# Performance work log

Hardware: AMD Instinct MI355X
Metric: run time of the kernel (lower is better)

Reference implementation:

```python
import jax, jax.numpy as jnp
import numpy as np

B, D, H = 16384, 1024, 1024
EPS = 1e-07


def setup_inputs() -> dict:
    key = jax.random.key(0)
    ks = jax.random.split(key, 16)
    s = 1.0 / np.sqrt(D)  # xavier-ish scale keeps exp() gate bounded
    mat = lambda k: (jax.random.normal(k, (D, H), dtype=jnp.float32) * s)
    zeros = lambda: jnp.zeros((H,), dtype=jnp.float32)
    return {
        "x": jax.random.normal(ks[0], (B, D), dtype=jnp.float32),
        "h_prev": jax.random.normal(ks[1], (B, H), dtype=jnp.float32) * 0.1,
        "c_prev": jax.random.normal(ks[2], (B, H), dtype=jnp.float32) * 0.1,
        "n_prev": jnp.ones((B, H), dtype=jnp.float32),
        "Wz": mat(ks[3]), "bWz": zeros(), "Rz": mat(ks[4]), "bRz": zeros(), "bz": zeros(),
        "Wi": mat(ks[5]), "bWi": zeros(), "Ri": mat(ks[6]), "bRi": zeros(), "bi": zeros(),
        "Wf": mat(ks[7]), "bWf": zeros(), "Rf": mat(ks[8]), "bRf": zeros(), "bf": zeros(),
        "Wo": mat(ks[9]), "bWo": zeros(), "Ro": mat(ks[10]), "bRo": zeros(), "bo": zeros(),
        "Wy": mat(ks[11]), "by": jnp.zeros((D,), dtype=jnp.float32),
    }


def reference(x, h_prev, c_prev, n_prev,
              Wz, bWz, Rz, bRz, bz,
              Wi, bWi, Ri, bRi, bi,
              Wf, bWf, Rf, bRf, bf,
              Wo, bWo, Ro, bRo, bo,
              Wy, by):
    # pre-activations: two fused GEMMs via concatenated weights
    Wcat = jnp.concatenate([Wz, Wi, Wf, Wo], axis=1)      # [D, 4H]
    Rcat = jnp.concatenate([Rz, Ri, Rf, Ro], axis=1)      # [H, 4H]
    bcat = jnp.concatenate([bWz + bRz + bz, bWi + bRi + bi,
                            bWf + bRf + bf, bWo + bRo + bo])
    pre = x @ Wcat + h_prev @ Rcat + bcat                  # [B, 4H]
    pz, pi, pf, po = jnp.split(pre, 4, axis=1)
    zt = jnp.tanh(pz)
    it = jnp.exp(pi)
    ft = jax.nn.sigmoid(pf)
    ot = jax.nn.sigmoid(po)
    C = ft * c_prev + it * zt
    n = ft * n_prev + it
    h = ot * jnp.tanh(C / (n + EPS))
    y = h @ Wy + by
    return y, (h, C, n)
```

## Files before the change

### kernel.cpp

```cpp
#include <hip/hip_runtime.h>
#include <math.h>
#include <stdint.h>


typedef __attribute__((ext_vector_type(8))) short bf16x8;
typedef __attribute__((ext_vector_type(4))) float f32x4;

constexpr int Bsz = 16384;
constexpr int Dd  = 1024;
constexpr int Hh  = 1024;
constexpr float EPSv = 1e-7f;

__device__ __forceinline__ unsigned short f2bf(float f) {
    union { float f; uint32_t u; } v; v.f = f;
    uint32_t u = v.u + 0x7fffu + ((v.u >> 16) & 1u);
    return (unsigned short)(u >> 16);
}

__device__ __forceinline__ void gload16(const void* g, void* l) {
    __builtin_amdgcn_global_load_lds(
        (const __attribute__((address_space(1))) void*)g,
        (__attribute__((address_space(3))) void*)l, 16, 0, 0);
}


__global__ __launch_bounds__(256)
void cvt_A(const float* __restrict__ x, const float* __restrict__ hp, unsigned short* __restrict__ A)
{
    const int idx = blockIdx.x * 256 + threadIdx.x;
    const int n = idx * 8;
    const int b = n >> 11, k = n & 2047;
    const float* s = (k < 1024) ? (x + (size_t)b * 1024 + k)
                                : (hp + (size_t)b * 1024 + (k - 1024));
    const float4 v0 = *(const float4*)s;
    const float4 v1 = *(const float4*)(s + 4);
    union { unsigned short u[8]; uint4 v; } pk;
    pk.u[0] = f2bf(v0.x); pk.u[1] = f2bf(v0.y); pk.u[2] = f2bf(v0.z); pk.u[3] = f2bf(v0.w);
    pk.u[4] = f2bf(v1.x); pk.u[5] = f2bf(v1.y); pk.u[6] = f2bf(v1.z); pk.u[7] = f2bf(v1.w);
    *(uint4*)(A + n) = pk.v;
}

__global__ __launch_bounds__(256)
void cvt_T(const float* __restrict__ src, unsigned short* __restrict__ dst,
           int ldd, int kbase, int g, int mode)
{
    __shared__ float tile[64][65];
    const int t = threadIdx.x;
    const int kt = blockIdx.x & 15, jt = blockIdx.x >> 4;
    {
        const int lr = t >> 4, lc = (t & 15) * 4;
        #pragma unroll
        for (int rr = 0; rr < 64; rr += 16) {
            const float4 v = *(const float4*)(src + (size_t)(kt * 64 + rr + lr) * 1024 + jt * 64 + lc);
            tile[rr + lr][lc + 0] = v.x;
            tile[rr + lr][lc + 1] = v.y;
            tile[rr + lr][lc + 2] = v.z;
            tile[rr + lr][lc + 3] = v.w;
        }
    }
    __syncthreads();
    const int jl = t >> 2, kc = (t & 3) * 16;
    const int j = jt * 64 + jl;
    const int cp = mode ? j : ((j & 15) | (g << 4) | ((j >> 4) << 6));
    union { unsigned short u[16]; uint4 v[2]; } pk;
    #pragma unroll
    for (int q = 0; q < 16; ++q) pk.u[q] = f2bf(tile[kc + q][jl]);
    uint4* d = (uint4*)(dst + (size_t)cp * ldd + kbase + kt * 64 + kc);
    d[0] = pk.v[0];
    d[1] = pk.v[1];
}

__global__ __launch_bounds__(256)
void bias_sum(const float* bWz, const float* bRz, const float* bz,
              const float* bWi, const float* bRi, const float* bi,
              const float* bWf, const float* bRf, const float* bf_,
              const float* bWo, const float* bRo, const float* bo,
              float* __restrict__ bs)
{
    const int j = blockIdx.x * 256 + threadIdx.x;
    bs[j]        = bWz[j] + bRz[j] + bz[j];
    bs[1024 + j] = bWi[j] + bRi[j] + bi[j];
    bs[2048 + j] = bWf[j] + bRf[j] + bf_[j];
    bs[3072 + j] = bWo[j] + bRo[j] + bo[j];
}


template<int LDA, int NT, int NTILES, class Epi>
__device__ void mfma_chain(const unsigned short* __restrict__ Ag,
                           const unsigned short* __restrict__ Bg,
                           int m0base, int n0, int t,
                           unsigned short* lds, Epi epi)
{
    constexpr int TOT = NT * NTILES;
    const int lane = t & 63, wid = t >> 6;
    const int wr = wid >> 2, wc = wid & 3;
    const int cl = lane & 15, hi = lane >> 4;
    const int aB = (wr * 128 + cl) * 64 + ((hi ^ (cl & 7)) << 3);
    const int bB = 16384 + (wc * 64 + cl) * 64 + ((hi ^ (cl & 7)) << 3);
    const int srow = t >> 3;
    const int schk = ((t & 7) ^ (srow & 7)) << 3;
    unsigned short* ldst = lds + t * 8;

    f32x4 acc[8][4];
    #pragma unroll
    for (int i = 0; i < 8; ++i)
        #pragma unroll
        for (int j = 0; j < 4; ++j) acc[i][j] = (f32x4)0.f;

    auto stgA = [&](int fi, int buf) {
        const int ot = fi / NT, kt = fi % NT;
        const unsigned short* g = Ag + (size_t)(m0base + ot * 256 + srow) * LDA + kt * 64 + schk;
        unsigned short* l = ldst + buf * 32768;
        gload16(g,                    l);
        gload16(g + (size_t) 64 * LDA, l + 4096);
        gload16(g + (size_t)128 * LDA, l + 8192);
        gload16(g + (size_t)192 * LDA, l + 12288);
    };
    auto stgB = [&](int fi, int buf) {
        const int kt = fi % NT;
        const unsigned short* g = Bg + (size_t)(n0 + srow) * LDA + kt * 64 + schk;
        unsigned short* l = ldst + buf * 32768 + 16384;
        gload16(g,                    l);
        gload16(g + (size_t) 64 * LDA, l + 4096);
        gload16(g + (size_t)128 * LDA, l + 8192);
        gload16(g + (size_t)192 * LDA, l + 12288);
    };

    stgA(0, 0); stgB(0, 0); stgB(1, 1);
    asm volatile("s_waitcnt vmcnt(4)" ::: "memory");
    __builtin_amdgcn_s_barrier();

    for (int fi = 0; fi < TOT; ++fi) {
        const int bufR = fi & 1;
        const unsigned short* L = lds + bufR * 32768;
        int f1 = fi + 1; if (f1 > TOT - 1) f1 = TOT - 1;
        int f2 = fi + 2; if (f2 > TOT - 1) f2 = TOT - 1;

        bf16x8 Br0[4], Br1[4], Ar00[4], Ar01[4], Ar10[4], Ar11[4];
        #pragma unroll
        for (int nn = 0; nn < 4; ++nn) Br0[nn]  = *(const bf16x8*)(L + (bB + nn * 1024));
        #pragma unroll
        for (int mm = 0; mm < 4; ++mm) Ar00[mm] = *(const bf16x8*)(L + (aB + mm * 1024));

        stgA(f1, bufR ^ 1);

        #pragma unroll
        for (int nn = 0; nn < 4; ++nn) Br1[nn]  = *(const bf16x8*)(L + ((bB + nn * 1024) ^ 32));
        #pragma unroll
        for (int mm = 0; mm < 4; ++mm) Ar01[mm] = *(const bf16x8*)(L + ((aB + mm * 1024) ^ 32));

        __builtin_amdgcn_s_setprio(1);
        #pragma unroll
        for (int mm = 0; mm < 4; ++mm)
            #pragma unroll
            for (int nn = 0; nn < 4; ++nn)
                acc[mm][nn] = __builtin_amdgcn_mfma_f32_16x16x32_bf16(Ar00[mm], Br0[nn], acc[mm][nn], 0, 0, 0);
        __builtin_amdgcn_s_setprio(0);

        #pragma unroll
        for (int mm = 0; mm < 4; ++mm) Ar10[mm] = *(const bf16x8*)(L + (aB + 4096 + mm * 1024));
        #pragma unroll
        for (int mm = 0; mm < 4; ++mm) Ar11[mm] = *(const bf16x8*)(L + ((aB + 4096 + mm * 1024) ^ 32));

        __builtin_amdgcn_s_setprio(1);
        #pragma unroll
        for (int mm = 0; mm < 4; ++mm)
            #pragma unroll
            for (int nn = 0; nn < 4; ++nn)
                acc[mm][nn] = __builtin_amdgcn_mfma_f32_16x16x32_bf16(Ar01[mm], Br1[nn], acc[mm][nn], 0, 0, 0);
        __builtin_amdgcn_s_setprio(0);

        __builtin_amdgcn_sched_barrier(0);
        __builtin_amdgcn_s_barrier();

        stgB(f2, bufR);

        __builtin_amdgcn_s_setprio(1);
        #pragma unroll
        for (int mm = 0; mm < 4; ++mm)
            #pragma unroll
            for (int nn = 0; nn < 4; ++nn)
                acc[4 + mm][nn] = __builtin_amdgcn_mfma_f32_16x16x32_bf16(Ar10[mm], Br0[nn], acc[4 + mm][nn], 0, 0, 0);
        __builtin_amdgcn_s_setprio(0);
        __builtin_amdgcn_s_setprio(1);
        #pragma unroll
        for (int mm = 0; mm < 4; ++mm)
            #pragma unroll
            for (int nn = 0; nn < 4; ++nn)
                acc[4 + mm][nn] = __builtin_amdgcn_mfma_f32_16x16x32_bf16(Ar11[mm], Br1[nn], acc[4 + mm][nn], 0, 0, 0);
        __builtin_amdgcn_s_setprio(0);

        __builtin_amdgcn_sched_barrier(0);
        asm volatile("s_waitcnt vmcnt(4)" ::: "memory");
        __builtin_amdgcn_s_barrier();

        if ((fi % NT) == NT - 1) {
            epi(fi / NT, acc);
            #pragma unroll
            for (int i = 0; i < 8; ++i)
                #pragma unroll
                for (int j = 0; j < 4; ++j) acc[i][j] = (f32x4)0.f;
        }
    }
    asm volatile("s_waitcnt vmcnt(0)" ::: "memory");
}

__global__ __launch_bounds__(512, 2)
void gemm_gates(const unsigned short* __restrict__ A, const unsigned short* __restrict__ WT,
                const float* __restrict__ bsum,
                const float* __restrict__ c_prev, const float* __restrict__ n_prev,
                float* __restrict__ out_h, float* __restrict__ out_C, float* __restrict__ out_n,
                unsigned short* __restrict__ h_bf)
{
    __shared__ unsigned short lds[65536];
    const int t = threadIdx.x;
    const int b = blockIdx.x;
    const int nb  = (b & 7) * 2 + (b >> 7);
    const int mb0 = ((b >> 3) & 15) * 4;
    const int m0base = mb0 * 256;
    const int n0 = nb * 256;

    const int lane = t & 63, wid = t >> 6;
    const int wr = wid >> 2, wc = wid & 3;
    const int cl = lane & 15, hi = lane >> 4;
    const int j_out = nb * 64 + wc * 16 + cl;
    const float bz_ = bsum[j_out];
    const float bi_ = bsum[1024 + j_out];
    const float bf_ = bsum[2048 + j_out];
    const float bo_ = bsum[3072 + j_out];

    auto epi = [&](int ot, f32x4 (&acc)[8][4]) {
        #pragma unroll
        for (int mf = 0; mf < 8; ++mf) {
            const int rb = m0base + ot * 256 + wr * 128 + mf * 16 + hi * 4;
            #pragma unroll
            for (int r = 0; r < 4; ++r) {
                const size_t idx = (size_t)(rb + r) * 1024 + j_out;
                const float pz = acc[mf][0][r] + bz_;
                const float pi = acc[mf][1][r] + bi_;
                const float pf = acc[mf][2][r] + bf_;
                const float po = acc[mf][3][r] + bo_;
                const float zt = tanhf(pz);
                const float it = expf(pi);
                const float ft = 1.f / (1.f + expf(-pf));
                const float ot_ = 1.f / (1.f + expf(-po));
                const float Cv = ft * c_prev[idx] + it * zt;
                const float nv = ft * n_prev[idx] + it;
                const float hv = ot_ * tanhf(Cv / (nv + EPSv));
                out_h[idx] = hv;
                out_C[idx] = Cv;
                out_n[idx] = nv;
                h_bf[idx] = f2bf(hv);
            }
        }
    };

    mfma_chain<2048, 32, 4>(A, WT, m0base, n0, t, lds, epi);
}

__global__ __launch_bounds__(512, 2)
void gemm_y(const unsigned short* __restrict__ A, const unsigned short* __restrict__ WyT,
            const float* __restrict__ by, float* __restrict__ y)
{
    __shared__ unsigned short lds[65536];
    const int t = threadIdx.x;
    const int b = blockIdx.x;
    const int nb = b & 3, mb = b >> 2;
    const int m0base = mb * 256, n0 = nb * 256;

    const int lane = t & 63, wid = t >> 6;
    const int wr = wid >> 2, wc = wid & 3;
    const int cl = lane & 15, hi = lane >> 4;

    auto epi = [&](int ot, f32x4 (&acc)[8][4]) {
        (void)ot;
        #pragma unroll
        for (int mf = 0; mf < 8; ++mf) {
            const int rb = m0base + wr * 128 + mf * 16 + hi * 4;
            #pragma unroll
            for (int nf = 0; nf < 4; ++nf) {
                const int c = n0 + wc * 64 + nf * 16 + cl;
                const float bc = by[c];
                #pragma unroll
                for (int r = 0; r < 4; ++r)
                    y[(size_t)(rb + r) * 1024 + c] = acc[mf][nf][r] + bc;
            }
        }
    };

    mfma_chain<1024, 16, 1>(A, WyT, m0base, n0, t, lds, epi);
}


constexpr int FBM = 64, FBN = 64, FBK = 16, FPAD = 4;

__global__ __launch_bounds__(256)
void fb_gates(const float* __restrict__ x, const float* __restrict__ h_prev,
              const float* __restrict__ c_prev, const float* __restrict__ n_prev,
              const float* __restrict__ Wz, const float* __restrict__ Rz,
              const float* __restrict__ Wi, const float* __restrict__ Ri,
              const float* __restrict__ Wf, const float* __restrict__ Rf,
              const float* __restrict__ Wo, const float* __restrict__ Ro,
              const float* __restrict__ bWz, const float* __restrict__ bRz, const float* __restrict__ bz,
              const float* __restrict__ bWi, const float* __restrict__ bRi, const float* __restrict__ bi,
              const float* __restrict__ bWf, const float* __restrict__ bRf, const float* __restrict__ bf_,
              const float* __restrict__ bWo, const float* __restrict__ bRo, const float* __restrict__ bo,
              float* __restrict__ out_h, float* __restrict__ out_C, float* __restrict__ out_n)
{
    __shared__ float sA[FBK][FBM + FPAD];
    __shared__ float sB[4][FBK][FBN + FPAD];
    const int t = threadIdx.x;
    const int col_blk = blockIdx.x & 15, row_blk = blockIdx.x >> 4;
    const int row0 = row_blk * FBM, col0 = col_blk * FBN;
    const int tx = t & 15, ty = t >> 4;
    float acc[4][4][4];
    #pragma unroll
    for (int g = 0; g < 4; ++g)
        for (int i = 0; i < 4; ++i)
            for (int j = 0; j < 4; ++j) acc[g][i][j] = 0.f;
    const int ar = t >> 2, ak = (t & 3) * 4, wk = t >> 4, wcc = (t & 15) * 4;
    for (int phase = 0; phase < 2; ++phase) {
        const float* Am = phase ? h_prev : x;
        const float* W0 = phase ? Rz : Wz; const float* W1 = phase ? Ri : Wi;
        const float* W2 = phase ? Rf : Wf; const float* W3 = phase ? Ro : Wo;
        for (int k0 = 0; k0 < 1024; k0 += FBK) {
            __syncthreads();
            {
                const float4 v = *(const float4*)(Am + (size_t)(row0 + ar) * 1024 + k0 + ak);
                sA[ak + 0][ar] = v.x; sA[ak + 1][ar] = v.y;
                sA[ak + 2][ar] = v.z; sA[ak + 3][ar] = v.w;
            }
            *(float4*)&sB[0][wk][wcc] = *(const float4*)(W0 + (size_t)(k0 + wk) * 1024 + col0 + wcc);
            *(float4*)&sB[1][wk][wcc] = *(const float4*)(W1 + (size_t)(k0 + wk) * 1024 + col0 + wcc);
            *(float4*)&sB[2][wk][wcc] = *(const float4*)(W2 + (size_t)(k0 + wk) * 1024 + col0 + wcc);
            *(float4*)&sB[3][wk][wcc] = *(const float4*)(W3 + (size_t)(k0 + wk) * 1024 + col0 + wcc);
            __syncthreads();
            #pragma unroll
            for (int kk = 0; kk < FBK; ++kk) {
                float a[4], bb[4][4];
                *(float4*)a = *(const float4*)&sA[kk][ty * 4];
                *(float4*)&bb[0][0] = *(const float4*)&sB[0][kk][tx * 4];
                *(float4*)&bb[1][0] = *(const float4*)&sB[1][kk][tx * 4];
                *(float4*)&bb[2][0] = *(const float4*)&sB[2][kk][tx * 4];
                *(float4*)&bb[3][0] = *(const float4*)&sB[3][kk][tx * 4];
                #pragma unroll
                for (int g = 0; g < 4; ++g)
                    for (int i = 0; i < 4; ++i)
                        for (int j = 0; j < 4; ++j)
                            acc[g][i][j] += a[i] * bb[g][j];
            }
        }
    }
    #pragma unroll
    for (int i = 0; i < 4; ++i) {
        const int r = row0 + ty * 4 + i;
        #pragma unroll
        for (int j = 0; j < 4; ++j) {
            const int c = col0 + tx * 4 + j;
            const float pz = acc[0][i][j] + bWz[c] + bRz[c] + bz[c];
            const float pi = acc[1][i][j] + bWi[c] + bRi[c] + bi[c];
            const float pf = acc[2][i][j] + bWf[c] + bRf[c] + bf_[c];
            const float po = acc[3][i][j] + bWo[c] + bRo[c] + bo[c];
            const float zt = tanhf(pz);
            const float it = expf(pi);
            const float ft = 1.f / (1.f + expf(-pf));
            const float ot = 1.f / (1.f + expf(-po));
            const size_t idx = (size_t)r * Hh + c;
            const float Cv = ft * c_prev[idx] + it * zt;
            const float nv = ft * n_prev[idx] + it;
            out_h[idx] = ot * tanhf(Cv / (nv + EPSv));
            out_C[idx] = Cv;
            out_n[idx] = nv;
        }
    }
}

__global__ __launch_bounds__(256)
void fb_ygemm(const float* __restrict__ hmat, const float* __restrict__ Wy,
              const float* __restrict__ by, float* __restrict__ y)
{
    __shared__ float sA[FBK][FBM + FPAD];
    __shared__ float sB[FBK][FBN + FPAD];
    const int t = threadIdx.x;
    const int col_blk = blockIdx.x & 15, row_blk = blockIdx.x >> 4;
    const int row0 = row_blk * FBM, col0 = col_blk * FBN;
    const int tx = t & 15, ty = t >> 4;
    float acc[4][4];
    #pragma unroll
    for (int i = 0; i < 4; ++i)
        for (int j = 0; j < 4; ++j) acc[i][j] = 0.f;
    const int ar = t >> 2, ak = (t & 3) * 4, wk = t >> 4, wcc = (t & 15) * 4;
    for (int k0 = 0; k0 < 1024; k0 += FBK) {
        __syncthreads();
        {
            const float4 v = *(const float4*)(hmat + (size_t)(row0 + ar) * 1024 + k0 + ak);
            sA[ak + 0][ar] = v.x; sA[ak + 1][ar] = v.y;
            sA[ak + 2][ar] = v.z; sA[ak + 3][ar] = v.w;
        }
        *(float4*)&sB[wk][wcc] = *(const float4*)(Wy + (size_t)(k0 + wk) * 1024 + col0 + wcc);
        __syncthreads();
        #pragma unroll
        for (int kk = 0; kk < FBK; ++kk) {
            float a[4], bb[4];
            *(float4*)a = *(const float4*)&sA[kk][ty * 4];
            *(float4*)bb = *(const float4*)&sB[kk][tx * 4];
            #pragma unroll
            for (int i = 0; i < 4; ++i)
                for (int j = 0; j < 4; ++j)
                    acc[i][j] += a[i] * bb[j];
        }
    }
    #pragma unroll
    for (int i = 0; i < 4; ++i) {
        const int r = row0 + ty * 4 + i;
        #pragma unroll
        for (int j = 0; j < 4; ++j) {
            const int c = col0 + tx * 4 + j;
            y[(size_t)r * Dd + c] = acc[i][j] + by[c];
        }
    }
}


extern "C" void kernel_launch(void* const* d_in, const int* in_sizes, int n_in,
                              void* d_out, int out_size, void* d_ws, size_t ws_size,
                              hipStream_t stream) {
    const float* x      = (const float*)d_in[0];
    const float* h_prev = (const float*)d_in[1];
    const float* c_prev = (const float*)d_in[2];
    const float* n_prev = (const float*)d_in[3];
    const float* Wz  = (const float*)d_in[4];
    const float* bWz = (const float*)d_in[5];
    const float* Rz  = (const float*)d_in[6];
    const float* bRz = (const float*)d_in[7];
    const float* bz  = (const float*)d_in[8];
    const float* Wi  = (const float*)d_in[9];
    const float* bWi = (const float*)d_in[10];
    const float* Ri  = (const float*)d_in[11];
    const float* bRi = (const float*)d_in[12];
    const float* bi  = (const float*)d_in[13];
    const float* Wf  = (const float*)d_in[14];
    const float* bWf = (const float*)d_in[15];
    const float* Rf  = (const float*)d_in[16];
    const float* bRf = (const float*)d_in[17];
    const float* bf_ = (const float*)d_in[18];
    const float* Wo  = (const float*)d_in[19];
    const float* bWo = (const float*)d_in[20];
    const float* Ro  = (const float*)d_in[21];
    const float* bRo = (const float*)d_in[22];
    const float* bo  = (const float*)d_in[23];
    const float* Wy  = (const float*)d_in[24];
    const float* by  = (const float*)d_in[25];

    float* y     = (float*)d_out;
    float* out_h = y + (size_t)Bsz * Dd;
    float* out_C = out_h + (size_t)Bsz * Hh;
    float* out_n = out_C + (size_t)Bsz * Hh;

    const size_t OFF_A    = 0;
    const size_t OFF_WT   = 67108864;
    const size_t OFF_WYT  = 83886080;
    const size_t OFF_HBF  = 85983232;
    const size_t OFF_BS   = 119537664;
    const size_t WS_NEED  = 119554048;

    if (ws_size >= WS_NEED) {
        char* ws = (char*)d_ws;
        unsigned short* A_bf = (unsigned short*)(ws + OFF_A);
        unsigned short* WT   = (unsigned short*)(ws + OFF_WT);
        unsigned short* WyT  = (unsigned short*)(ws + OFF_WYT);
        unsigned short* h_bf = (unsigned short*)(ws + OFF_HBF);
        float* bsum          = (float*)(ws + OFF_BS);

        cvt_A<<<16384, 256, 0, stream>>>(x, h_prev, A_bf);
        cvt_T<<<256, 256, 0, stream>>>(Wz, WT, 2048, 0,    0, 0);
        cvt_T<<<256, 256, 0, stream>>>(Rz, WT, 2048, 1024, 0, 0);
        cvt_T<<<256, 256, 0, stream>>>(Wi, WT, 2048, 0,    1, 0);
        cvt_T<<<256, 256, 0, stream>>>(Ri, WT, 2048, 1024, 1, 0);
        cvt_T<<<256, 256, 0, stream>>>(Wf, WT, 2048, 0,    2, 0);
        cvt_T<<<256, 256, 0, stream>>>(Rf, WT, 2048, 1024, 2, 0);
        cvt_T<<<256, 256, 0, stream>>>(Wo, WT, 2048, 0,    3, 0);
        cvt_T<<<256, 256, 0, stream>>>(Ro, WT, 2048, 1024, 3, 0);
        cvt_T<<<256, 256, 0, stream>>>(Wy, WyT, 1024, 0,   0, 1);
        bias_sum<<<4, 256, 0, stream>>>(bWz, bRz, bz, bWi, bRi, bi,
                                        bWf, bRf, bf_, bWo, bRo, bo, bsum);

        gemm_gates<<<256, 512, 0, stream>>>(A_bf, WT, bsum, c_prev, n_prev,
                                            out_h, out_C, out_n, h_bf);
        gemm_y<<<256, 512, 0, stream>>>(h_bf, WyT, by, y);
    } else {
        dim3 block(256);
        dim3 grid((Bsz / FBM) * (Hh / FBN));
        fb_gates<<<grid, block, 0, stream>>>(x, h_prev, c_prev, n_prev,
                                             Wz, Rz, Wi, Ri, Wf, Rf, Wo, Ro,
                                             bWz, bRz, bz, bWi, bRi, bi,
                                             bWf, bRf, bf_, bWo, bRo, bo,
                                             out_h, out_C, out_n);
        fb_ygemm<<<grid, block, 0, stream>>>(out_h, Wy, by, y);
    }
}
```

Baseline: 451.4 us.

## Switch GEMM core to 32x32x16 MFMA with triple-buffered B tiles

Replaces the 16x16x32 bf16 MFMA mainloop with a 32x32x16 variant. The wave layout changes to 4x2, each wave owns a 64x128 tile, and the gate-weight column permutation and epilogue indexing are updated to match. B tiles are now triple-buffered in a larger LDS allocation. The loop is split into four barrier-delimited phases that interleave LDS reads, global-to-LDS prefetch and MFMA bursts, and the gate epilogue uses __expf-based tanh and sigmoid. The goal is fewer LDS reads per FLOP and higher MFMA throughput. The cost is more LDS per block, which may hurt occupancy, more barriers, and slightly lower-precision transcendentals.

```diff
diff --git a/kernel.cpp b/kernel.cpp
--- a/kernel.cpp
+++ b/kernel.cpp
@@ -5,6 +5,7 @@
 
 typedef __attribute__((ext_vector_type(8))) short bf16x8;
 typedef __attribute__((ext_vector_type(4))) float f32x4;
+typedef __attribute__((ext_vector_type(16))) float f32x16;
 
 constexpr int Bsz = 16384;
 constexpr int Dd  = 1024;
@@ -21,6 +22,14 @@
     __builtin_amdgcn_global_load_lds(
         (const __attribute__((address_space(1))) void*)g,
         (__attribute__((address_space(3))) void*)l, 16, 0, 0);
+}
+
+__device__ __forceinline__ float sigm_f(float x) { return 1.f / (1.f + __expf(-x)); }
+__device__ __forceinline__ float tanh_f(float x) {
+    const float ax = fabsf(x);
+    const float t = __expf(-2.f * ax);
+    const float r = (1.f - t) / (1.f + t);
+    return copysignf(r, x);
 }
 
 
@@ -61,7 +70,7 @@
     __syncthreads();
     const int jl = t >> 2, kc = (t & 3) * 16;
     const int j = jt * 64 + jl;
-    const int cp = mode ? j : ((j & 15) | (g << 4) | ((j >> 4) << 6));
+    const int cp = mode ? j : ((j & 31) | (g << 5) | ((j >> 5) << 7));
     union { unsigned short u[16]; uint4 v[2]; } pk;
     #pragma unroll
     for (int q = 0; q < 16; ++q) pk.u[q] = f2bf(tile[kc + q][jl]);
@@ -85,122 +94,127 @@
 }
 
 
-template<int LDA, int NT, int NTILES, class Epi>
-__device__ void mfma_chain(const unsigned short* __restrict__ Ag,
-                           const unsigned short* __restrict__ Bg,
-                           int m0base, int n0, int t,
-                           unsigned short* lds, Epi epi)
-{
-    constexpr int TOT = NT * NTILES;
+#define PH_PRE() { __builtin_amdgcn_sched_barrier(0); __builtin_amdgcn_s_barrier(); \
+    asm volatile("s_waitcnt lgkmcnt(0)" ::: "memory"); __builtin_amdgcn_sched_barrier(0); \
+    __builtin_amdgcn_s_setprio(1); }
+#define PH_POST() { __builtin_amdgcn_s_setprio(0); __builtin_amdgcn_sched_barrier(0); \
+    __builtin_amdgcn_s_barrier(); }
+#define MFMA32(d, a, b) d = __builtin_amdgcn_mfma_f32_32x32x16_bf16(a, b, d, 0, 0, 0)
+
+template<int LD, int NTK_LOG2, int NTILES, class Epi>
+__device__ void mfma32_chain(const unsigned short* __restrict__ Ag,
+                             const unsigned short* __restrict__ Bg,
+                             int m0base, int n0, int t,
+                             unsigned short* lds, Epi epi)
+{
+    constexpr int NTK = 1 << NTK_LOG2;
+    constexpr int TOT = NTK * NTILES;
     const int lane = t & 63, wid = t >> 6;
-    const int wr = wid >> 2, wc = wid & 3;
-    const int cl = lane & 15, hi = lane >> 4;
-    const int aB = (wr * 128 + cl) * 64 + ((hi ^ (cl & 7)) << 3);
-    const int bB = 16384 + (wc * 64 + cl) * 64 + ((hi ^ (cl & 7)) << 3);
+    const int wr = wid >> 1, wc = wid & 1;
+    const int l31 = lane & 31, hi5 = lane >> 5, e7 = l31 & 7;
+    const int rA0 = wr * 64 + l31;
+    const int rB0 = wc * 128 + l31;
     const int srow = t >> 3;
-    const int schk = ((t & 7) ^ (srow & 7)) << 3;
-    unsigned short* ldst = lds + t * 8;
-
-    f32x4 acc[8][4];
+    const int schk = ((t & 7) ^ (srow & 7)) * 8;
+    const int ldst8 = t * 8;
+
+    f32x16 acc[2][4];
     #pragma unroll
-    for (int i = 0; i < 8; ++i)
-        #pragma unroll
-        for (int j = 0; j < 4; ++j) acc[i][j] = (f32x4)0.f;
-
-    auto stgA = [&](int fi, int buf) {
-        const int ot = fi / NT, kt = fi % NT;
-        const unsigned short* g = Ag + (size_t)(m0base + ot * 256 + srow) * LDA + kt * 64 + schk;
-        unsigned short* l = ldst + buf * 32768;
-        gload16(g,                    l);
-        gload16(g + (size_t) 64 * LDA, l + 4096);
-        gload16(g + (size_t)128 * LDA, l + 8192);
-        gload16(g + (size_t)192 * LDA, l + 12288);
+    for (int i = 0; i < 2; ++i)
+        #pragma unroll
+        for (int j = 0; j < 4; ++j) acc[i][j] = (f32x16)0.f;
+
+    auto stgA = [&](int f, int h, int buf) {
+        const int ot = f >> NTK_LOG2, kt = f & (NTK - 1);
+        const unsigned short* g = Ag + (size_t)(m0base + ot * 256 + h * 128 + srow) * LD + kt * 64 + schk;
+        unsigned short* l = lds + buf * 16384 + h * 8192 + ldst8;
+        gload16(g,                 l);
+        gload16(g + (size_t)64 * LD, l + 4096);
     };
-    auto stgB = [&](int fi, int buf) {
-        const int kt = fi % NT;
-        const unsigned short* g = Bg + (size_t)(n0 + srow) * LDA + kt * 64 + schk;
-        unsigned short* l = ldst + buf * 32768 + 16384;
-        gload16(g,                    l);
-        gload16(g + (size_t) 64 * LDA, l + 4096);
-        gload16(g + (size_t)128 * LDA, l + 8192);
-        gload16(g + (size_t)192 * LDA, l + 12288);
+    auto stgB = [&](int f, int h, int buf) {
+        const int kt = f & (NTK - 1);
+        const unsigned short* g = Bg + (size_t)(n0 + h * 128 + srow) * LD + kt * 64 + schk;
+        unsigned short* l = lds + 32768 + buf * 16384 + h * 8192 + ldst8;
+        gload16(g,                 l);
+        gload16(g + (size_t)64 * LD, l + 4096);
     };
-
-    stgA(0, 0); stgB(0, 0); stgB(1, 1);
+    auto rdA = [&](int buf, int mi, int ks) {
+        return *(const bf16x8*)(lds + buf * 16384 + (rA0 + mi * 32) * 64 + ((((ks << 1) + hi5) ^ e7) << 3));
+    };
+    auto rdB = [&](int buf, int nn, int ks) {
+        return *(const bf16x8*)(lds + 32768 + buf * 16384 + (rB0 + nn * 32) * 64 + ((((ks << 1) + hi5) ^ e7) << 3));
+    };
+
+    stgA(0, 0, 0); stgA(0, 1, 0);
+    stgB(0, 0, 0); stgB(0, 1, 0);
+    stgB(1, 0, 1); stgB(1, 1, 1);
     asm volatile("s_waitcnt vmcnt(4)" ::: "memory");
     __builtin_amdgcn_s_barrier();
 
-    for (int fi = 0; fi < TOT; ++fi) {
-        const int bufR = fi & 1;
-        const unsigned short* L = lds + bufR * 32768;
-        int f1 = fi + 1; if (f1 > TOT - 1) f1 = TOT - 1;
-        int f2 = fi + 2; if (f2 > TOT - 1) f2 = TOT - 1;
-
-        bf16x8 Br0[4], Br1[4], Ar00[4], Ar01[4], Ar10[4], Ar11[4];
-        #pragma unroll
-        for (int nn = 0; nn < 4; ++nn) Br0[nn]  = *(const bf16x8*)(L + (bB + nn * 1024));
-        #pragma unroll
-        for (int mm = 0; mm < 4; ++mm) Ar00[mm] = *(const bf16x8*)(L + (aB + mm * 1024));
-
-        stgA(f1, bufR ^ 1);
-
-        #pragma unroll
-        for (int nn = 0; nn < 4; ++nn) Br1[nn]  = *(const bf16x8*)(L + ((bB + nn * 1024) ^ 32));
-        #pragma unroll
-        for (int mm = 0; mm < 4; ++mm) Ar01[mm] = *(const bf16x8*)(L + ((aB + mm * 1024) ^ 32));
-
-        __builtin_amdgcn_s_setprio(1);
-        #pragma unroll
-        for (int mm = 0; mm < 4; ++mm)
-            #pragma unroll
-            for (int nn = 0; nn < 4; ++nn)
-                acc[mm][nn] = __builtin_amdgcn_mfma_f32_16x16x32_bf16(Ar00[mm], Br0[nn], acc[mm][nn], 0, 0, 0);
+    int bB = 0;
+    for (int f = 0; f < TOT; ++f) {
+        const int bA = f & 1;
+        int f1 = f + 1; if (f1 > TOT - 1) f1 = TOT - 1;
+        int f2 = f + 2; if (f2 > TOT - 1) f2 = TOT - 1;
+        const int bB2 = (bB >= 1) ? (bB - 1) : 2;
+
+        bf16x8 a00, a01, a10, a11, b00, b01, b10, b11, c00, c01, c10, c11;
+
+        a00 = rdA(bA, 0, 0); a10 = rdA(bA, 1, 0);
+        a01 = rdA(bA, 0, 1); a11 = rdA(bA, 1, 1);
+        b00 = rdB(bB, 0, 0); b10 = rdB(bB, 1, 0);
+        b01 = rdB(bB, 0, 1); b11 = rdB(bB, 1, 1);
+        stgA(f1, 0, bA ^ 1);
+        PH_PRE();
+        MFMA32(acc[0][0], a00, b00); MFMA32(acc[1][0], a10, b00);
+        MFMA32(acc[0][1], a00, b10); MFMA32(acc[1][1], a10, b10);
+        MFMA32(acc[0][0], a01, b01); MFMA32(acc[1][0], a11, b01);
+        MFMA32(acc[0][1], a01, b11); MFMA32(acc[1][1], a11, b11);
+        PH_POST();
+
+        c00 = rdB(bB, 2, 0); c10 = rdB(bB, 3, 0);
+        c01 = rdB(bB, 2, 1); c11 = rdB(bB, 3, 1);
+        stgA(f1, 1, bA ^ 1);
+        PH_PRE();
+        MFMA32(acc[0][2], a00, c00); MFMA32(acc[1][2], a10, c00);
+        MFMA32(acc[0][3], a00, c10); MFMA32(acc[1][3], a10, c10);
+        MFMA32(acc[0][2], a01, c01); MFMA32(acc[1][2], a11, c01);
+        MFMA32(acc[0][3], a01, c11); MFMA32(acc[1][3], a11, c11);
+        PH_POST();
+
+        a00 = rdA(bA, 0, 2); a10 = rdA(bA, 1, 2);
+        a01 = rdA(bA, 0, 3); a11 = rdA(bA, 1, 3);
+        b00 = rdB(bB, 0, 2); b10 = rdB(bB, 1, 2);
+        b01 = rdB(bB, 0, 3); b11 = rdB(bB, 1, 3);
+        stgB(f2, 0, bB2);
+        PH_PRE();
+        MFMA32(acc[0][0], a00, b00); MFMA32(acc[1][0], a10, b00);
+        MFMA32(acc[0][1], a00, b10); MFMA32(acc[1][1], a10, b10);
+        MFMA32(acc[0][0], a01, b01); MFMA32(acc[1][0], a11, b01);
+        MFMA32(acc[0][1], a01, b11); MFMA32(acc[1][1], a11, b11);
+        PH_POST();
+
+        c00 = rdB(bB, 2, 2); c10 = rdB(bB, 3, 2);
+        c01 = rdB(bB, 2, 3); c11 = rdB(bB, 3, 3);
+        stgB(f2, 1, bB2);
+        PH_PRE();
+        MFMA32(acc[0][2], a00, c00); MFMA32(acc[1][2], a10, c00);
+        MFMA32(acc[0][3], a00, c10); MFMA32(acc[1][3], a10, c10);
+        MFMA32(acc[0][2], a01, c01); MFMA32(acc[1][2], a11, c01);
+        MFMA32(acc[0][3], a01, c11); MFMA32(acc[1][3], a11, c11);
         __builtin_amdgcn_s_setprio(0);
-
-        #pragma unroll
-        for (int mm = 0; mm < 4; ++mm) Ar10[mm] = *(const bf16x8*)(L + (aB + 4096 + mm * 1024));
-        #pragma unroll
-        for (int mm = 0; mm < 4; ++mm) Ar11[mm] = *(const bf16x8*)(L + ((aB + 4096 + mm * 1024) ^ 32));
-
-        __builtin_amdgcn_s_setprio(1);
-        #pragma unroll
-        for (int mm = 0; mm < 4; ++mm)
-            #pragma unroll
-            for (int nn = 0; nn < 4; ++nn)
-                acc[mm][nn] = __builtin_amdgcn_mfma_f32_16x16x32_bf16(Ar01[mm], Br1[nn], acc[mm][nn], 0, 0, 0);
-        __builtin_amdgcn_s_setprio(0);
-
-        __builtin_amdgcn_sched_barrier(0);
-        __builtin_amdgcn_s_barrier();
-
-        stgB(f2, bufR);
-
-        __builtin_amdgcn_s_setprio(1);
-        #pragma unroll
-        for (int mm = 0; mm < 4; ++mm)
-            #pragma unroll
-            for (int nn = 0; nn < 4; ++nn)
-                acc[4 + mm][nn] = __builtin_amdgcn_mfma_f32_16x16x32_bf16(Ar10[mm], Br0[nn], acc[4 + mm][nn], 0, 0, 0);
-        __builtin_amdgcn_s_setprio(0);
-        __builtin_amdgcn_s_setprio(1);
-        #pragma unroll
-        for (int mm = 0; mm < 4; ++mm)
-            #pragma unroll
-            for (int nn = 0; nn < 4; ++nn)
-                acc[4 + mm][nn] = __builtin_amdgcn_mfma_f32_16x16x32_bf16(Ar11[mm], Br1[nn], acc[4 + mm][nn], 0, 0, 0);
-        __builtin_amdgcn_s_setprio(0);
-
         __builtin_amdgcn_sched_barrier(0);
         asm volatile("s_waitcnt vmcnt(4)" ::: "memory");
         __builtin_amdgcn_s_barrier();
 
-        if ((fi % NT) == NT - 1) {
-            epi(fi / NT, acc);
+        if ((f & (NTK - 1)) == NTK - 1) {
+            epi(f >> NTK_LOG2, acc);
             #pragma unroll
-            for (int i = 0; i < 8; ++i)
+            for (int i = 0; i < 2; ++i)
                 #pragma unroll
-                for (int j = 0; j < 4; ++j) acc[i][j] = (f32x4)0.f;
-        }
+                for (int j = 0; j < 4; ++j) acc[i][j] = (f32x16)0.f;
+        }
+        bB = (bB == 2) ? 0 : bB + 1;
     }
     asm volatile("s_waitcnt vmcnt(0)" ::: "memory");
 }
@@ -212,7 +226,7 @@
                 float* __restrict__ out_h, float* __restrict__ out_C, float* __restrict__ out_n,
                 unsigned short* __restrict__ h_bf)
 {
-    __shared__ unsigned short lds[65536];
+    __shared__ unsigned short lds[81920];
     const int t = threadIdx.x;
     const int b = blockIdx.x;
     const int nb  = (b & 7) * 2 + (b >> 7);
@@ -221,32 +235,33 @@
     const int n0 = nb * 256;
 
     const int lane = t & 63, wid = t >> 6;
-    const int wr = wid >> 2, wc = wid & 3;
-    const int cl = lane & 15, hi = lane >> 4;
-    const int j_out = nb * 64 + wc * 16 + cl;
+    const int wr = wid >> 1, wc = wid & 1;
+    const int l31 = lane & 31, hi5 = lane >> 5;
+    const int j_out = (nb * 2 + wc) * 32 + l31;
     const float bz_ = bsum[j_out];
     const float bi_ = bsum[1024 + j_out];
     const float bf_ = bsum[2048 + j_out];
     const float bo_ = bsum[3072 + j_out];
 
-    auto epi = [&](int ot, f32x4 (&acc)[8][4]) {
-        #pragma unroll
-        for (int mf = 0; mf < 8; ++mf) {
-            const int rb = m0base + ot * 256 + wr * 128 + mf * 16 + hi * 4;
+    auto epi = [&](int ot, f32x16 (&acc)[2][4]) {
+        #pragma unroll
+        for (int mi = 0; mi < 2; ++mi) {
+            const int rbase = m0base + ot * 256 + wr * 64 + mi * 32 + 4 * hi5;
             #pragma unroll
-            for (int r = 0; r < 4; ++r) {
-                const size_t idx = (size_t)(rb + r) * 1024 + j_out;
-                const float pz = acc[mf][0][r] + bz_;
-                const float pi = acc[mf][1][r] + bi_;
-                const float pf = acc[mf][2][r] + bf_;
-                const float po = acc[mf][3][r] + bo_;
-                const float zt = tanhf(pz);
-                const float it = expf(pi);
-                const float ft = 1.f / (1.f + expf(-pf));
-                const float ot_ = 1.f / (1.f + expf(-po));
+            for (int r = 0; r < 16; ++r) {
+                const int row = rbase + (r & 3) + 8 * (r >> 2);
+                const size_t idx = (size_t)row * 1024 + j_out;
+                const float pz = acc[mi][0][r] + bz_;
+                const float pi = acc[mi][1][r] + bi_;
+                const float pf = acc[mi][2][r] + bf_;
+                const float po = acc[mi][3][r] + bo_;
+                const float zt = tanh_f(pz);
+                const float it = __expf(pi);
+                const float ft = sigm_f(pf);
+                const float ot_ = sigm_f(po);
                 const float Cv = ft * c_prev[idx] + it * zt;
                 const float nv = ft * n_prev[idx] + it;
-                const float hv = ot_ * tanhf(Cv / (nv + EPSv));
+                const float hv = ot_ * tanh_f(Cv / (nv + EPSv));
                 out_h[idx] = hv;
                 out_C[idx] = Cv;
                 out_n[idx] = nv;
@@ -255,40 +270,42 @@
         }
     };
 
-    mfma_chain<2048, 32, 4>(A, WT, m0base, n0, t, lds, epi);
+    mfma32_chain<2048, 5, 4>(A, WT, m0base, n0, t, lds, epi);
 }
 
 __global__ __launch_bounds__(512, 2)
 void gemm_y(const unsigned short* __restrict__ A, const unsigned short* __restrict__ WyT,
             const float* __restrict__ by, float* __restrict__ y)
 {
-    __shared__ unsigned short lds[65536];
+    __shared__ unsigned short lds[81920];
     const int t = threadIdx.x;
     const int b = blockIdx.x;
     const int nb = b & 3, mb = b >> 2;
     const int m0base = mb * 256, n0 = nb * 256;
 
     const int lane = t & 63, wid = t >> 6;
-    const int wr = wid >> 2, wc = wid & 3;
-    const int cl = lane & 15, hi = lane >> 4;
-
-    auto epi = [&](int ot, f32x4 (&acc)[8][4]) {
+    const int wr = wid >> 1, wc = wid & 1;
+    const int l31 = lane & 31, hi5 = lane >> 5;
+
+    auto epi = [&](int ot, f32x16 (&acc)[2][4]) {
         (void)ot;
         #pragma unroll
-        for (int mf = 0; mf < 8; ++mf) {
-            const int rb = m0base + wr * 128 + mf * 16 + hi * 4;
+        for (int mi = 0; mi < 2; ++mi) {
+            const int rbase = m0base + wr * 64 + mi * 32 + 4 * hi5;
             #pragma unroll
-            for (int nf = 0; nf < 4; ++nf) {
-                const int c = n0 + wc * 64 + nf * 16 + cl;
+            for (int nn = 0; nn < 4; ++nn) {
+                const int c = n0 + wc * 128 + nn * 32 + l31;
                 const float bc = by[c];
                 #pragma unroll
-                for (int r = 0; r < 4; ++r)
-                    y[(size_t)(rb + r) * 1024 + c] = acc[mf][nf][r] + bc;
+                for (int r = 0; r < 16; ++r) {
+                    const int row = rbase + (r & 3) + 8 * (r >> 2);
+                    y[(size_t)row * 1024 + c] = acc[mi][nn][r] + bc;
+                }
             }
         }
     };
 
-    mfma_chain<1024, 16, 1>(A, WyT, m0base, n0, t, lds, epi);
+    mfma32_chain<1024, 4, 1>(A, WyT, m0base, n0, t, lds, epi);
 }
 
 
```

Result: slower. 468.1 us (+3.7%).

## Restructure MFMA mainloop with triple-buffered B tiles and fast transcendental epilogue

Applied to the files above, without the earlier changes.

Rewrites the GEMM core loop so the A tile is double-buffered and the B tile triple-buffered, with one barrier per iteration, prefetches issued at the top, and a simpler load-then-MFMA sequence without priority hints. LDS grows to 160KB per block. The gate epilogue also swaps tanhf/expf for __expf-based fast sigmoid and tanh approximations. The larger LDS footprint may reduce occupancy below the declared two blocks per CU, and the simpler schedule loses the hand-tuned interleaving of LDS reads with MFMAs.

```diff
diff --git a/kernel.cpp b/kernel.cpp
--- a/kernel.cpp
+++ b/kernel.cpp
@@ -21,6 +21,14 @@
     __builtin_amdgcn_global_load_lds(
         (const __attribute__((address_space(1))) void*)g,
         (__attribute__((address_space(3))) void*)l, 16, 0, 0);
+}
+
+__device__ __forceinline__ float sigm_f(float x) { return 1.f / (1.f + __expf(-x)); }
+__device__ __forceinline__ float tanh_f(float x) {
+    const float ax = fabsf(x);
+    const float t = __expf(-2.f * ax);
+    const float r = (1.f - t) / (1.f + t);
+    return copysignf(r, x);
 }
 
 
@@ -85,21 +93,41 @@
 }
 
 
-template<int LDA, int NT, int NTILES, class Epi>
-__device__ void mfma_chain(const unsigned short* __restrict__ Ag,
-                           const unsigned short* __restrict__ Bg,
-                           int m0base, int n0, int t,
-                           unsigned short* lds, Epi epi)
-{
-    constexpr int TOT = NT * NTILES;
+template<int LD, int NTK, int NTILES, class Epi>
+__device__ void mfma_core(const unsigned short* __restrict__ Ag,
+                          const unsigned short* __restrict__ Bg,
+                          int m0base, int n0, int t,
+                          unsigned short* lds, Epi epi)
+{
+    constexpr int TOT = NTK * NTILES;
     const int lane = t & 63, wid = t >> 6;
     const int wr = wid >> 2, wc = wid & 3;
     const int cl = lane & 15, hi = lane >> 4;
-    const int aB = (wr * 128 + cl) * 64 + ((hi ^ (cl & 7)) << 3);
-    const int bB = 16384 + (wc * 64 + cl) * 64 + ((hi ^ (cl & 7)) << 3);
+    char* const L = (char*)lds;
+    const int rdA0 = (wr * 128 + cl) * 128 + ((hi ^ (cl & 7)) << 4);
+    const int rdB0 = 65536 + (wc * 64 + cl) * 128 + ((hi ^ (cl & 7)) << 4);
     const int srow = t >> 3;
-    const int schk = ((t & 7) ^ (srow & 7)) << 3;
-    unsigned short* ldst = lds + t * 8;
+    const int schk = ((t & 7) ^ (srow & 7)) * 8;
+    const int sdst = t * 16;
+
+    auto stgA = [&](int f, int buf) {
+        const int ot = f / NTK, kt = f % NTK;
+        const unsigned short* g = Ag + (size_t)(m0base + ot * 256 + srow) * LD + kt * 64 + schk;
+        char* d = L + buf * 32768 + sdst;
+        gload16(g,                  d);
+        gload16(g + (size_t) 64 * LD, d + 8192);
+        gload16(g + (size_t)128 * LD, d + 16384);
+        gload16(g + (size_t)192 * LD, d + 24576);
+    };
+    auto stgB = [&](int f, int buf) {
+        const int kt = f % NTK;
+        const unsigned short* g = Bg + (size_t)(n0 + srow) * LD + kt * 64 + schk;
+        char* d = L + 65536 + buf * 32768 + sdst;
+        gload16(g,                  d);
+        gload16(g + (size_t) 64 * LD, d + 8192);
+        gload16(g + (size_t)128 * LD, d + 16384);
+        gload16(g + (size_t)192 * LD, d + 24576);
+    };
 
     f32x4 acc[8][4];
     #pragma unroll
@@ -107,100 +135,52 @@
         #pragma unroll
         for (int j = 0; j < 4; ++j) acc[i][j] = (f32x4)0.f;
 
-    auto stgA = [&](int fi, int buf) {
-        const int ot = fi / NT, kt = fi % NT;
-        const unsigned short* g = Ag + (size_t)(m0base + ot * 256 + srow) * LDA + kt * 64 + schk;
-        unsigned short* l = ldst + buf * 32768;
-        gload16(g,                    l);
-        gload16(g + (size_t) 64 * LDA, l + 4096);
-        gload16(g + (size_t)128 * LDA, l + 8192);
-        gload16(g + (size_t)192 * LDA, l + 12288);
-    };
-    auto stgB = [&](int fi, int buf) {
-        const int kt = fi % NT;
-        const unsigned short* g = Bg + (size_t)(n0 + srow) * LDA + kt * 64 + schk;
-        unsigned short* l = ldst + buf * 32768 + 16384;
-        gload16(g,                    l);
-        gload16(g + (size_t) 64 * LDA, l + 4096);
-        gload16(g + (size_t)128 * LDA, l + 8192);
-        gload16(g + (size_t)192 * LDA, l + 12288);
-    };
-
     stgA(0, 0); stgB(0, 0); stgB(1, 1);
-    asm volatile("s_waitcnt vmcnt(4)" ::: "memory");
-    __builtin_amdgcn_s_barrier();
-
-    for (int fi = 0; fi < TOT; ++fi) {
-        const int bufR = fi & 1;
-        const unsigned short* L = lds + bufR * 32768;
-        int f1 = fi + 1; if (f1 > TOT - 1) f1 = TOT - 1;
-        int f2 = fi + 2; if (f2 > TOT - 1) f2 = TOT - 1;
-
-        bf16x8 Br0[4], Br1[4], Ar00[4], Ar01[4], Ar10[4], Ar11[4];
-        #pragma unroll
-        for (int nn = 0; nn < 4; ++nn) Br0[nn]  = *(const bf16x8*)(L + (bB + nn * 1024));
-        #pragma unroll
-        for (int mm = 0; mm < 4; ++mm) Ar00[mm] = *(const bf16x8*)(L + (aB + mm * 1024));
-
-        stgA(f1, bufR ^ 1);
-
-        #pragma unroll
-        for (int nn = 0; nn < 4; ++nn) Br1[nn]  = *(const bf16x8*)(L + ((bB + nn * 1024) ^ 32));
-        #pragma unroll
-        for (int mm = 0; mm < 4; ++mm) Ar01[mm] = *(const bf16x8*)(L + ((aB + mm * 1024) ^ 32));
-
-        __builtin_amdgcn_s_setprio(1);
-        #pragma unroll
-        for (int mm = 0; mm < 4; ++mm)
-            #pragma unroll
-            for (int nn = 0; nn < 4; ++nn)
-                acc[mm][nn] = __builtin_amdgcn_mfma_f32_16x16x32_bf16(Ar00[mm], Br0[nn], acc[mm][nn], 0, 0, 0);
-        __builtin_amdgcn_s_setprio(0);
-
-        #pragma unroll
-        for (int mm = 0; mm < 4; ++mm) Ar10[mm] = *(const bf16x8*)(L + (aB + 4096 + mm * 1024));
-        #pragma unroll
-        for (int mm = 0; mm < 4; ++mm) Ar11[mm] = *(const bf16x8*)(L + ((aB + 4096 + mm * 1024) ^ 32));
-
-        __builtin_amdgcn_s_setprio(1);
-        #pragma unroll
-        for (int mm = 0; mm < 4; ++mm)
-            #pragma unroll
-            for (int nn = 0; nn < 4; ++nn)
-                acc[mm][nn] = __builtin_amdgcn_mfma_f32_16x16x32_bf16(Ar01[mm], Br1[nn], acc[mm][nn], 0, 0, 0);
-        __builtin_amdgcn_s_setprio(0);
-
-        __builtin_amdgcn_sched_barrier(0);
+
+    int bA = 0, bB = 0;
+    for (int f = 0; f < TOT; ++f) {
+        const int f1 = (f + 1 < TOT) ? f + 1 : TOT - 1;
+        const int f2 = (f + 2 < TOT) ? f + 2 : TOT - 1;
+        const int bB2 = (bB >= 1) ? bB - 1 : 2;
+
         __builtin_amdgcn_s_barrier();
-
-        stgB(f2, bufR);
-
-        __builtin_amdgcn_s_setprio(1);
-        #pragma unroll
-        for (int mm = 0; mm < 4; ++mm)
-            #pragma unroll
-            for (int nn = 0; nn < 4; ++nn)
-                acc[4 + mm][nn] = __builtin_amdgcn_mfma_f32_16x16x32_bf16(Ar10[mm], Br0[nn], acc[4 + mm][nn], 0, 0, 0);
-        __builtin_amdgcn_s_setprio(0);
-        __builtin_amdgcn_s_setprio(1);
-        #pragma unroll
-        for (int mm = 0; mm < 4; ++mm)
-            #pragma unroll
-            for (int nn = 0; nn < 4; ++nn)
-                acc[4 + mm][nn] = __builtin_amdgcn_mfma_f32_16x16x32_bf16(Ar11[mm], Br1[nn], acc[4 + mm][nn], 0, 0, 0);
-        __builtin_amdgcn_s_setprio(0);
-
-        __builtin_amdgcn_sched_barrier(0);
-        asm volatile("s_waitcnt vmcnt(4)" ::: "memory");
-        __builtin_amdgcn_s_barrier();
-
-        if ((fi % NT) == NT - 1) {
-            epi(fi / NT, acc);
+        stgA(f1, bA ^ 1);
+        stgB(f2, bB2);
+        asm volatile("s_waitcnt vmcnt(12)" ::: "memory");
+
+        const int aof = rdA0 + (bA << 15);
+        const int bof = rdB0 + (bB << 15);
+        bf16x8 a[8], b[4];
+
+        #pragma unroll
+        for (int mf = 0; mf < 8; ++mf) a[mf] = *(const bf16x8*)(L + aof + mf * 2048);
+        #pragma unroll
+        for (int nf = 0; nf < 4; ++nf) b[nf] = *(const bf16x8*)(L + bof + nf * 2048);
+        #pragma unroll
+        for (int mf = 0; mf < 8; ++mf)
+            #pragma unroll
+            for (int nf = 0; nf < 4; ++nf)
+                acc[mf][nf] = __builtin_amdgcn_mfma_f32_16x16x32_bf16(a[mf], b[nf], acc[mf][nf], 0, 0, 0);
+
+        #pragma unroll
+        for (int mf = 0; mf < 8; ++mf) a[mf] = *(const bf16x8*)(L + (aof ^ 64) + mf * 2048);
+        #pragma unroll
+        for (int nf = 0; nf < 4; ++nf) b[nf] = *(const bf16x8*)(L + (bof ^ 64) + nf * 2048);
+        #pragma unroll
+        for (int mf = 0; mf < 8; ++mf)
+            #pragma unroll
+            for (int nf = 0; nf < 4; ++nf)
+                acc[mf][nf] = __builtin_amdgcn_mfma_f32_16x16x32_bf16(a[mf], b[nf], acc[mf][nf], 0, 0, 0);
+
+        if ((f % NTK) == NTK - 1) {
+            epi(f / NTK, acc);
             #pragma unroll
             for (int i = 0; i < 8; ++i)
                 #pragma unroll
                 for (int j = 0; j < 4; ++j) acc[i][j] = (f32x4)0.f;
         }
+        bA ^= 1;
+        bB = (bB == 2) ? 0 : bB + 1;
     }
     asm volatile("s_waitcnt vmcnt(0)" ::: "memory");
 }
@@ -212,7 +192,7 @@
                 float* __restrict__ out_h, float* __restrict__ out_C, float* __restrict__ out_n,
                 unsigned short* __restrict__ h_bf)
 {
-    __shared__ unsigned short lds[65536];
+    __shared__ unsigned short lds[81920];
     const int t = threadIdx.x;
     const int b = blockIdx.x;
     const int nb  = (b & 7) * 2 + (b >> 7);
@@ -240,13 +220,13 @@
                 const float pi = acc[mf][1][r] + bi_;
                 const float pf = acc[mf][2][r] + bf_;
                 const float po = acc[mf][3][r] + bo_;
-                const float zt = tanhf(pz);
-                const float it = expf(pi);
-                const float ft = 1.f / (1.f + expf(-pf));
-                const float ot_ = 1.f / (1.f + expf(-po));
+                const float zt = tanh_f(pz);
+                const float it = __expf(pi);
+                const float ft = sigm_f(pf);
+                const float ot_ = sigm_f(po);
                 const float Cv = ft * c_prev[idx] + it * zt;
                 const float nv = ft * n_prev[idx] + it;
-                const float hv = ot_ * tanhf(Cv / (nv + EPSv));
+                const float hv = ot_ * tanh_f(Cv / (nv + EPSv));
                 out_h[idx] = hv;
                 out_C[idx] = Cv;
                 out_n[idx] = nv;
@@ -255,14 +235,14 @@
         }
     };
 
-    mfma_chain<2048, 32, 4>(A, WT, m0base, n0, t, lds, epi);
+    mfma_core<2048, 32, 4>(A, WT, m0base, n0, t, lds, epi);
 }
 
 __global__ __launch_bounds__(512, 2)
 void gemm_y(const unsigned short* __restrict__ A, const unsigned short* __restrict__ WyT,
             const float* __restrict__ by, float* __restrict__ y)
 {
-    __shared__ unsigned short lds[65536];
+    __shared__ unsigned short lds[81920];
     const int t = threadIdx.x;
     const int b = blockIdx.x;
     const int nb = b & 3, mb = b >> 2;
@@ -288,7 +268,7 @@
         }
     };
 
-    mfma_chain<1024, 16, 1>(A, WyT, m0base, n0, t, lds, epi);
+    mfma_core<1024, 16, 1>(A, WyT, m0base, n0, t, lds, epi);
 }
 
 
```

New measurement: 439.0 us. 2.8% less time.
